# Kernel tuning notes

Measured on AMD Instinct MI355X. Metric: run time of the kernel, lower is better.

The kernel has to match this reference:

```python
import jax, jax.numpy as jnp
import numpy as np
import math

B, S, KV, D, H = 4, 512, 4096, 1024, 16
HD = D // H  # head_dim = 64


def setup_inputs() -> dict:
    key = jax.random.key(0)
    ks = jax.random.split(key, 12)
    scale = 0.02
    return {
        "x": jax.random.normal(ks[0], (B, S, D), dtype=jnp.float32),
        "xa": jax.random.normal(ks[1], (B, KV, D), dtype=jnp.float32),
        "Wq": jax.random.normal(ks[2], (D, D), dtype=jnp.float32) * scale,
        "bq": jax.random.normal(ks[3], (D,), dtype=jnp.float32) * scale,
        "Wk": jax.random.normal(ks[4], (D, D), dtype=jnp.float32) * scale,  # key has no bias
        "Wv": jax.random.normal(ks[5], (D, D), dtype=jnp.float32) * scale,
        "bv": jax.random.normal(ks[6], (D,), dtype=jnp.float32) * scale,
        "Wo": jax.random.normal(ks[7], (D, D), dtype=jnp.float32) * scale,
        "bo": jax.random.normal(ks[8], (D,), dtype=jnp.float32) * scale,
        "cache_k": jnp.zeros((B, H, KV, HD), dtype=jnp.float32),
        "cache_v": jnp.zeros((B, H, KV, HD), dtype=jnp.float32),
    }


def reference(x, xa, Wq, bq, Wk, Wv, bv, Wo, bo, cache_k, cache_v):
    bsz, seq_len, _ = x.shape
    kv_len = xa.shape[1]
    # projections (torch nn.Linear convention: y = x @ W^T + b)
    q = (x @ Wq.T + bq).reshape(bsz, seq_len, H, HD).transpose(0, 2, 1, 3)   # [B,H,S,HD]
    k = (xa @ Wk.T).reshape(bsz, kv_len, H, HD).transpose(0, 2, 1, 3)        # [B,H,KV,HD]
    v = (xa @ Wv.T + bv).reshape(bsz, kv_len, H, HD).transpose(0, 2, 1, 3)   # [B,H,KV,HD]
    # prefill path: scatter k/v into positions [0, kv_len) of the cache
    updated_k = cache_k.at[:, :, :kv_len, :].set(k)
    updated_v = cache_v.at[:, :, :kv_len, :].set(v)
    # attention over full cache, fp32 softmax as in the original
    scores = jnp.einsum('bhqd,bhkd->bhqk', q, updated_k) / math.sqrt(HD)
    probs = jax.nn.softmax(scores.astype(jnp.float32), axis=-1).astype(q.dtype)
    attn = jnp.einsum('bhqk,bhkd->bhqd', probs, updated_v)                   # [B,H,S,HD]
    attn = attn.transpose(0, 2, 1, 3).reshape(bsz, seq_len, H * HD)
    out = attn @ Wo.T + bo
    return out, updated_k, updated_v
```

## Files before the change

### kernel.cpp

```cpp
#include <hip/hip_runtime.h>
#include <hip/hip_bf16.h>

using u16 = unsigned short;
typedef __bf16 bf16x8 __attribute__((ext_vector_type(8)));
typedef float f32x4 __attribute__((ext_vector_type(4)));

#define SB 4
#define SS 512
#define SKV 4096
#define SD 1024
#define SH 16
#define SHD 64
#define NSPLIT 4
#define NROWS 32768

__device__ inline u16 f2bf(float f){
  __hip_bfloat16 h = __float2bfloat16(f);
  return __builtin_bit_cast(u16, h);
}

__device__ inline bf16x8 ld_frag_g(const u16* p){
  uint4 v = *reinterpret_cast<const uint4*>(p);
  return __builtin_bit_cast(bf16x8, v);
}

__device__ inline bf16x8 ld_frag_lds(const char* base, int ob){
  uint4 v = *reinterpret_cast<const uint4*>(base + ob);
  return __builtin_bit_cast(bf16x8, v);
}

__global__ __launch_bounds__(256) void cast_kernel(const float* __restrict__ src,
                                                   u16* __restrict__ dst, int n4){
  int i = blockIdx.x * 256 + threadIdx.x;
  if (i < n4){
    float4 f = reinterpret_cast<const float4*>(src)[i];
    ushort4 u;
    u.x = f2bf(f.x); u.y = f2bf(f.y); u.z = f2bf(f.z); u.w = f2bf(f.w);
    reinterpret_cast<ushort4*>(dst)[i] = u;
  }
}

enum { MODE_Q = 0, MODE_K = 1, MODE_V = 2, MODE_OUT = 3 };

template<int MODE>
__global__ __launch_bounds__(256) void gemm_bt(const u16* __restrict__ A,
                                               const u16* __restrict__ W,
                                               const float* __restrict__ bias,
                                               float* __restrict__ outF,
                                               u16* __restrict__ outB)
{
  __shared__ u16 As[128*64];
  __shared__ u16 Bs[128*64];
  const int tid  = threadIdx.x;
  const int lane = tid & 63;
  const int wm   = ((tid >> 6) >> 1) * 64;
  const int wn   = ((tid >> 6) & 1) * 64;
  const long rowBase = (long)blockIdx.x * 128;
  const long colBase = (long)blockIdx.y * 128;

  f32x4 acc[4][4];
#pragma unroll
  for (int i = 0; i < 4; i++)
#pragma unroll
    for (int j = 0; j < 4; j++)
      acc[i][j] = (f32x4){0.f, 0.f, 0.f, 0.f};

  for (int kt = 0; kt < 16; ++kt){
    __syncthreads();
#pragma unroll
    for (int i = 0; i < 4; i++){
      int u = tid + i * 256;
      int r = u >> 3, c = u & 7;
      uint4 va = *reinterpret_cast<const uint4*>(A + (rowBase + r) * 1024 + kt * 64 + c * 8);
      uint4 vw = *reinterpret_cast<const uint4*>(W + (colBase + r) * 1024 + kt * 64 + c * 8);
      int ob = (r * 128 + c * 16) ^ ((r & 7) << 4);
      *reinterpret_cast<uint4*>(reinterpret_cast<char*>(As) + ob) = va;
      *reinterpret_cast<uint4*>(reinterpret_cast<char*>(Bs) + ob) = vw;
    }
    __syncthreads();
#pragma unroll
    for (int kk = 0; kk < 2; kk++){
      bf16x8 af[4], bfr[4];
#pragma unroll
      for (int mi = 0; mi < 4; mi++){
        int row = wm + mi * 16 + (lane & 15);
        int ob = (row * 128 + kk * 64 + (lane >> 4) * 16) ^ ((row & 7) << 4);
        af[mi] = __builtin_bit_cast(bf16x8,
                 *reinterpret_cast<const uint4*>(reinterpret_cast<const char*>(As) + ob));
      }
#pragma unroll
      for (int ni = 0; ni < 4; ni++){
        int row = wn + ni * 16 + (lane & 15);
        int ob = (row * 128 + kk * 64 + (lane >> 4) * 16) ^ ((row & 7) << 4);
        bfr[ni] = __builtin_bit_cast(bf16x8,
                 *reinterpret_cast<const uint4*>(reinterpret_cast<const char*>(Bs) + ob));
      }
#pragma unroll
      for (int mi = 0; mi < 4; mi++)
#pragma unroll
        for (int ni = 0; ni < 4; ni++)
          acc[mi][ni] = __builtin_amdgcn_mfma_f32_16x16x32_bf16(af[mi], bfr[ni], acc[mi][ni], 0, 0, 0);
    }
  }

#pragma unroll
  for (int mi = 0; mi < 4; mi++){
#pragma unroll
    for (int ni = 0; ni < 4; ni++){
      long gn = colBase + wn + ni * 16 + (lane & 15);
      float bb = 0.f;
      if (MODE == MODE_Q || MODE == MODE_V || MODE == MODE_OUT) bb = bias[gn];
      if (MODE == MODE_V){
        long gmBase = rowBase + wm + mi * 16 + ((lane >> 4) << 2);
        long b = gmBase >> 12, kv = gmBase & 4095;
        long h = gn >> 6, hd = gn & 63;
        long fidx = ((b * SH + h) * SKV + kv) * SHD + hd;
        ushort4 pk;
        float v0 = acc[mi][ni][0] + bb; outF[fidx          ] = v0; pk.x = f2bf(v0);
        float v1 = acc[mi][ni][1] + bb; outF[fidx +     SHD] = v1; pk.y = f2bf(v1);
        float v2 = acc[mi][ni][2] + bb; outF[fidx + 2 * SHD] = v2; pk.z = f2bf(v2);
        float v3 = acc[mi][ni][3] + bb; outF[fidx + 3 * SHD] = v3; pk.w = f2bf(v3);
        *reinterpret_cast<ushort4*>(outB + ((b * SH + h) * SHD + hd) * SKV + kv) = pk;
      } else {
#pragma unroll
        for (int r = 0; r < 4; r++){
          long gm = rowBase + wm + mi * 16 + ((lane >> 4) << 2) + r;
          float val = acc[mi][ni][r] + bb;
          if (MODE == MODE_OUT){
            outF[gm * 1024 + gn] = val;
          } else if (MODE == MODE_Q){
            long b = gm >> 9, s = gm & 511;
            long h = gn >> 6, hd = gn & 63;
            outB[((b * SH + h) * SS + s) * SHD + hd] = f2bf(val);
          } else {
            long b = gm >> 12, kv = gm & 4095;
            long h = gn >> 6, hd = gn & 63;
            long idx = ((b * SH + h) * SKV + kv) * SHD + hd;
            outF[idx] = val;
            outB[idx] = f2bf(val);
          }
        }
      }
    }
  }
}

__global__ __launch_bounds__(256) void attn_partial(const u16* __restrict__ qb,
                                                    const u16* __restrict__ kb,
                                                    const u16* __restrict__ vTb,
                                                    float* __restrict__ opart,
                                                    float* __restrict__ ml){
  __shared__ u16 Klds[64 * 64];
  __shared__ u16 Vlds[64 * 64];
  __shared__ u16 PT[4][16 * 72];
  const int tid  = threadIdx.x;
  const int lane = tid & 63;
  const int wid  = tid >> 6;
  const int c    = lane & 15;
  const int hi   = lane >> 4;
  const long bh  = blockIdx.x;
  const int  qt  = blockIdx.y;
  const int  split = blockIdx.z;

  const u16* qp = qb + (bh * SS + qt * 64 + wid * 16 + c) * SHD + hi * 8;
  const bf16x8 bq0 = ld_frag_g(qp);
  const bf16x8 bq1 = ld_frag_g(qp + 32);

  f32x4 acc[4];
#pragma unroll
  for (int i = 0; i < 4; i++) acc[i] = (f32x4){0.f, 0.f, 0.f, 0.f};
  float mrun = -INFINITY, lrun = 0.f;

  const u16* kbase = kb  + bh * SKV * SHD;
  const u16* vbase = vTb + bh * SHD * SKV;
  u16* pt = &PT[wid][0];
  char* kch = reinterpret_cast<char*>(Klds);
  char* vch = reinterpret_cast<char*>(Vlds);

  for (int kt = split * 16; kt < split * 16 + 16; ++kt){
    __syncthreads();
#pragma unroll
    for (int i = 0; i < 2; i++){
      int u = tid + i * 256;
      int r = u >> 3, cc = u & 7;
      uint4 kv4 = *reinterpret_cast<const uint4*>(kbase + (kt * 64 + r) * SHD + cc * 8);
      uint4 vv4 = *reinterpret_cast<const uint4*>(vbase + (long)r * SKV + kt * 64 + cc * 8);
      int ob = (r * 128 + cc * 16) ^ ((r & 7) << 4);
      *reinterpret_cast<uint4*>(kch + ob) = kv4;
      *reinterpret_cast<uint4*>(vch + ob) = vv4;
    }
    __syncthreads();

    f32x4 sT[4];
#pragma unroll
    for (int ni = 0; ni < 4; ni++){
      int krow = ni * 16 + c;
      int swz = (krow & 7) << 4;
      int a0 = (krow * 128 + hi * 16) ^ swz;
      int a1 = (krow * 128 + 64 + hi * 16) ^ swz;
      f32x4 z = (f32x4){0.f, 0.f, 0.f, 0.f};
      sT[ni] = __builtin_amdgcn_mfma_f32_16x16x32_bf16(ld_frag_lds(kch, a0), bq0, z, 0, 0, 0);
      sT[ni] = __builtin_amdgcn_mfma_f32_16x16x32_bf16(ld_frag_lds(kch, a1), bq1, sT[ni], 0, 0, 0);
      sT[ni] *= 0.125f;
    }
    f32x4 mv = __builtin_elementwise_max(__builtin_elementwise_max(sT[0], sT[1]),
                                         __builtin_elementwise_max(sT[2], sT[3]));
    float t = fmaxf(fmaxf(mv[0], mv[1]), fmaxf(mv[2], mv[3]));
    t = fmaxf(t, __shfl_xor(t, 16));
    t = fmaxf(t, __shfl_xor(t, 32));
    float mn = fmaxf(mrun, t);
    float al = __expf(mrun - mn);
    f32x4 psv = (f32x4){0.f, 0.f, 0.f, 0.f};
#pragma unroll
    for (int ni = 0; ni < 4; ni++){
      f32x4 p;
      p[0] = __expf(sT[ni][0] - mn); p[1] = __expf(sT[ni][1] - mn);
      p[2] = __expf(sT[ni][2] - mn); p[3] = __expf(sT[ni][3] - mn);
      psv += p;
      ushort4 pk;
      pk.x = f2bf(p[0]); pk.y = f2bf(p[1]); pk.z = f2bf(p[2]); pk.w = f2bf(p[3]);
      *reinterpret_cast<ushort4*>(pt + c * 72 + ni * 16 + hi * 4) = pk;
    }
    float ps = (psv[0] + psv[1]) + (psv[2] + psv[3]);
    ps += __shfl_xor(ps, 16);
    ps += __shfl_xor(ps, 32);
    lrun = lrun * al + ps;
    mrun = mn;
#pragma unroll
    for (int ni = 0; ni < 4; ni++) acc[ni] *= al;
#pragma unroll
    for (int m = 0; m < 2; m++){
      bf16x8 pfrag = __builtin_bit_cast(bf16x8,
          *reinterpret_cast<const uint4*>(pt + c * 72 + m * 32 + hi * 8));
#pragma unroll
      for (int ni = 0; ni < 4; ni++){
        int vrow = ni * 16 + c;
        int av = (vrow * 128 + m * 64 + hi * 16) ^ ((vrow & 7) << 4);
        acc[ni] = __builtin_amdgcn_mfma_f32_16x16x32_bf16(ld_frag_lds(vch, av), pfrag, acc[ni], 0, 0, 0);
      }
    }
  }

  const long row = bh * SS + (long)qt * 64 + wid * 16 + c;
  float* ob = opart + ((long)split * NROWS + row) * SHD;
#pragma unroll
  for (int ni = 0; ni < 4; ni++)
    *reinterpret_cast<f32x4*>(ob + ni * 16 + hi * 4) = acc[ni];
  if (hi == 0){
    ml[(long)split * NROWS + row] = mrun;
    ml[(long)NSPLIT * NROWS + (long)split * NROWS + row] = lrun;
  }
}

__global__ __launch_bounds__(256) void attn_combine(const float* __restrict__ opart,
                                                    const float* __restrict__ ml,
                                                    u16* __restrict__ attnb){
  long idx4 = (long)blockIdx.x * 256 + threadIdx.x;
  long row = idx4 >> 4;
  int  c   = (int)(idx4 & 15);
  float m0 = ml[row], m1 = ml[NROWS + row], m2 = ml[2L*NROWS + row], m3 = ml[3L*NROWS + row];
  float M = fmaxf(fmaxf(m0, m1), fmaxf(m2, m3));
  float w0 = __expf(m0 - M), w1 = __expf(m1 - M), w2 = __expf(m2 - M), w3 = __expf(m3 - M);
  const float* lb = ml + (long)NSPLIT * NROWS;
  float L = w0*lb[row] + w1*lb[NROWS+row] + w2*lb[2L*NROWS+row] + w3*lb[3L*NROWS+row];
  float inv = 1.f / L;
  const float4* op = reinterpret_cast<const float4*>(opart);
  float4 v0 = op[(0L*NROWS + row) * 16 + c];
  float4 v1 = op[(1L*NROWS + row) * 16 + c];
  float4 v2 = op[(2L*NROWS + row) * 16 + c];
  float4 v3 = op[(3L*NROWS + row) * 16 + c];
  float4 val;
  val.x = (w0*v0.x + w1*v1.x + w2*v2.x + w3*v3.x) * inv;
  val.y = (w0*v0.y + w1*v1.y + w2*v2.y + w3*v3.y) * inv;
  val.z = (w0*v0.z + w1*v1.z + w2*v2.z + w3*v3.z) * inv;
  val.w = (w0*v0.w + w1*v1.w + w2*v2.w + w3*v3.w) * inv;
  long bh = row >> 9, s = row & 511;
  long b = bh >> 4, h = bh & 15;
  ushort4 u;
  u.x = f2bf(val.x); u.y = f2bf(val.y); u.z = f2bf(val.z); u.w = f2bf(val.w);
  reinterpret_cast<ushort4*>(attnb)[((b * SS + s) * SD + h * SHD) / 4 + c] = u;
}

extern "C" void kernel_launch(void* const* d_in, const int* in_sizes, int n_in,
                              void* d_out, int out_size, void* d_ws, size_t ws_size,
                              hipStream_t stream)
{
  const float* x  = (const float*)d_in[0];
  const float* xa = (const float*)d_in[1];
  const float* Wq = (const float*)d_in[2];
  const float* bq = (const float*)d_in[3];
  const float* Wk = (const float*)d_in[4];
  const float* Wv = (const float*)d_in[5];
  const float* bv = (const float*)d_in[6];
  const float* Wo = (const float*)d_in[7];
  const float* bo = (const float*)d_in[8];

  float* outO = (float*)d_out;
  float* outK = outO + (long)SB * SS * SD;
  float* outV = outK + (long)SB * SH * SKV * SHD;

  u16* ws   = (u16*)d_ws;
  u16* xb   = ws;
  u16* xab  = xb   + 2097152L;
  u16* Wqb  = xab  + 16777216L;
  u16* Wkb  = Wqb  + 1048576L;
  u16* Wvb  = Wkb  + 1048576L;
  u16* Wob  = Wvb  + 1048576L;
  u16* qbuf = Wob  + 1048576L;
  u16* kbuf = qbuf + 2097152L;
  u16* vTbuf= kbuf + 16777216L;
  u16* mlb  = vTbuf+ 16777216L;

  u16*   attnb = xb;
  float* opart = (float*)xab;
  float* ml    = (float*)mlb;

  auto cast_launch = [&](const float* s, u16* d, long n){
    int n4 = (int)(n / 4);
    cast_kernel<<<(n4 + 255) / 256, 256, 0, stream>>>(s, d, n4);
  };
  cast_launch(x,  xb,  2097152L);
  cast_launch(xa, xab, 16777216L);
  cast_launch(Wq, Wqb, 1048576L);
  cast_launch(Wk, Wkb, 1048576L);
  cast_launch(Wv, Wvb, 1048576L);
  cast_launch(Wo, Wob, 1048576L);

  gemm_bt<MODE_Q>  <<<dim3(16, 8),  256, 0, stream>>>(xb,  Wqb, bq, nullptr, qbuf);
  gemm_bt<MODE_K>  <<<dim3(128, 8), 256, 0, stream>>>(xab, Wkb, nullptr, outK, kbuf);
  gemm_bt<MODE_V>  <<<dim3(128, 8), 256, 0, stream>>>(xab, Wvb, bv, outV, vTbuf);
  attn_partial     <<<dim3(64, 8, NSPLIT), 256, 0, stream>>>(qbuf, kbuf, vTbuf, opart, ml);
  attn_combine     <<<2048, 256, 0, stream>>>(opart, ml, attnb);
  gemm_bt<MODE_OUT><<<dim3(16, 8),  256, 0, stream>>>(attnb, Wob, bo, outO, nullptr);
}
```

Measured before the change: 275.0 us.

## Fuse K and V projections into one GEMM and fold softmax scale into Q

Replaces the separate K and V projection GEMMs with a single kernel that loads each xa tile once and computes both outputs with two accumulator sets. It also folds the 1/sqrt(HD) scale and log2(e) into the Q projection so attention can use exp2f without a per-score multiply. The goal is to halve the reads of the large bf16 xa activation and trim ALU work in the softmax loop. In exchange the fused kernel doubles its accumulator registers and LDS footprint, which may lower occupancy, and pre-scaling Q before the bf16 cast slightly changes rounding.

Measured after the change: 301.4 us. +9.6%, slower.

```diff
diff --git a/kernel.cpp b/kernel.cpp
--- a/kernel.cpp
+++ b/kernel.cpp
@@ -13,6 +13,7 @@
 #define SHD 64
 #define NSPLIT 4
 #define NROWS 32768
+#define QSCALE 0.18033688011112042f
 
 __device__ inline u16 f2bf(float f){
   __hip_bfloat16 h = __float2bfloat16(f);
@@ -40,7 +41,7 @@
   }
 }
 
-enum { MODE_Q = 0, MODE_K = 1, MODE_V = 2, MODE_OUT = 3 };
+enum { MODE_Q = 0, MODE_OUT = 3 };
 
 template<int MODE>
 __global__ __launch_bounds__(256) void gemm_bt(const u16* __restrict__ A,
@@ -85,15 +86,13 @@
       for (int mi = 0; mi < 4; mi++){
         int row = wm + mi * 16 + (lane & 15);
         int ob = (row * 128 + kk * 64 + (lane >> 4) * 16) ^ ((row & 7) << 4);
-        af[mi] = __builtin_bit_cast(bf16x8,
-                 *reinterpret_cast<const uint4*>(reinterpret_cast<const char*>(As) + ob));
+        af[mi] = ld_frag_lds(reinterpret_cast<const char*>(As), ob);
       }
 #pragma unroll
       for (int ni = 0; ni < 4; ni++){
         int row = wn + ni * 16 + (lane & 15);
         int ob = (row * 128 + kk * 64 + (lane >> 4) * 16) ^ ((row & 7) << 4);
-        bfr[ni] = __builtin_bit_cast(bf16x8,
-                 *reinterpret_cast<const uint4*>(reinterpret_cast<const char*>(Bs) + ob));
+        bfr[ni] = ld_frag_lds(reinterpret_cast<const char*>(Bs), ob);
       }
 #pragma unroll
       for (int mi = 0; mi < 4; mi++)
@@ -108,39 +107,117 @@
 #pragma unroll
     for (int ni = 0; ni < 4; ni++){
       long gn = colBase + wn + ni * 16 + (lane & 15);
-      float bb = 0.f;
-      if (MODE == MODE_Q || MODE == MODE_V || MODE == MODE_OUT) bb = bias[gn];
-      if (MODE == MODE_V){
-        long gmBase = rowBase + wm + mi * 16 + ((lane >> 4) << 2);
-        long b = gmBase >> 12, kv = gmBase & 4095;
-        long h = gn >> 6, hd = gn & 63;
-        long fidx = ((b * SH + h) * SKV + kv) * SHD + hd;
-        ushort4 pk;
-        float v0 = acc[mi][ni][0] + bb; outF[fidx          ] = v0; pk.x = f2bf(v0);
-        float v1 = acc[mi][ni][1] + bb; outF[fidx +     SHD] = v1; pk.y = f2bf(v1);
-        float v2 = acc[mi][ni][2] + bb; outF[fidx + 2 * SHD] = v2; pk.z = f2bf(v2);
-        float v3 = acc[mi][ni][3] + bb; outF[fidx + 3 * SHD] = v3; pk.w = f2bf(v3);
-        *reinterpret_cast<ushort4*>(outB + ((b * SH + h) * SHD + hd) * SKV + kv) = pk;
-      } else {
-#pragma unroll
-        for (int r = 0; r < 4; r++){
-          long gm = rowBase + wm + mi * 16 + ((lane >> 4) << 2) + r;
-          float val = acc[mi][ni][r] + bb;
-          if (MODE == MODE_OUT){
-            outF[gm * 1024 + gn] = val;
-          } else if (MODE == MODE_Q){
-            long b = gm >> 9, s = gm & 511;
-            long h = gn >> 6, hd = gn & 63;
-            outB[((b * SH + h) * SS + s) * SHD + hd] = f2bf(val);
-          } else {
-            long b = gm >> 12, kv = gm & 4095;
-            long h = gn >> 6, hd = gn & 63;
-            long idx = ((b * SH + h) * SKV + kv) * SHD + hd;
-            outF[idx] = val;
-            outB[idx] = f2bf(val);
-          }
+      float bb = bias[gn];
+#pragma unroll
+      for (int r = 0; r < 4; r++){
+        long gm = rowBase + wm + mi * 16 + ((lane >> 4) << 2) + r;
+        float val = acc[mi][ni][r] + bb;
+        if (MODE == MODE_OUT){
+          outF[gm * 1024 + gn] = val;
+        } else {
+          long b = gm >> 9, s = gm & 511;
+          long h = gn >> 6, hd = gn & 63;
+          outB[((b * SH + h) * SS + s) * SHD + hd] = f2bf(val * QSCALE);
         }
       }
+    }
+  }
+}
+
+__global__ __launch_bounds__(256) void gemm_kv(const u16* __restrict__ A,
+                                               const u16* __restrict__ Wk,
+                                               const u16* __restrict__ Wv,
+                                               const float* __restrict__ bv,
+                                               float* __restrict__ outK,
+                                               u16* __restrict__ outKb,
+                                               float* __restrict__ outV,
+                                               u16* __restrict__ outVTb)
+{
+  __shared__ u16 As [128*64];
+  __shared__ u16 Bks[128*64];
+  __shared__ u16 Bvs[128*64];
+  const int tid  = threadIdx.x;
+  const int lane = tid & 63;
+  const int wm   = ((tid >> 6) >> 1) * 64;
+  const int wn   = ((tid >> 6) & 1) * 64;
+  const long rowBase = (long)blockIdx.x * 128;
+  const long colBase = (long)blockIdx.y * 128;
+
+  f32x4 accK[4][4], accV[4][4];
+#pragma unroll
+  for (int i = 0; i < 4; i++)
+#pragma unroll
+    for (int j = 0; j < 4; j++){
+      accK[i][j] = (f32x4){0.f, 0.f, 0.f, 0.f};
+      accV[i][j] = (f32x4){0.f, 0.f, 0.f, 0.f};
+    }
+
+  for (int kt = 0; kt < 16; ++kt){
+    __syncthreads();
+#pragma unroll
+    for (int i = 0; i < 4; i++){
+      int u = tid + i * 256;
+      int r = u >> 3, c = u & 7;
+      uint4 va = *reinterpret_cast<const uint4*>(A  + (rowBase + r) * 1024 + kt * 64 + c * 8);
+      uint4 vk = *reinterpret_cast<const uint4*>(Wk + (colBase + r) * 1024 + kt * 64 + c * 8);
+      uint4 vv = *reinterpret_cast<const uint4*>(Wv + (colBase + r) * 1024 + kt * 64 + c * 8);
+      int ob = (r * 128 + c * 16) ^ ((r & 7) << 4);
+      *reinterpret_cast<uint4*>(reinterpret_cast<char*>(As)  + ob) = va;
+      *reinterpret_cast<uint4*>(reinterpret_cast<char*>(Bks) + ob) = vk;
+      *reinterpret_cast<uint4*>(reinterpret_cast<char*>(Bvs) + ob) = vv;
+    }
+    __syncthreads();
+#pragma unroll
+    for (int kk = 0; kk < 2; kk++){
+      bf16x8 af[4], bk[4], bvf[4];
+#pragma unroll
+      for (int mi = 0; mi < 4; mi++){
+        int row = wm + mi * 16 + (lane & 15);
+        int ob = (row * 128 + kk * 64 + (lane >> 4) * 16) ^ ((row & 7) << 4);
+        af[mi] = ld_frag_lds(reinterpret_cast<const char*>(As), ob);
+      }
+#pragma unroll
+      for (int ni = 0; ni < 4; ni++){
+        int row = wn + ni * 16 + (lane & 15);
+        int ob = (row * 128 + kk * 64 + (lane >> 4) * 16) ^ ((row & 7) << 4);
+        bk[ni]  = ld_frag_lds(reinterpret_cast<const char*>(Bks), ob);
+        bvf[ni] = ld_frag_lds(reinterpret_cast<const char*>(Bvs), ob);
+      }
+#pragma unroll
+      for (int mi = 0; mi < 4; mi++)
+#pragma unroll
+        for (int ni = 0; ni < 4; ni++){
+          accK[mi][ni] = __builtin_amdgcn_mfma_f32_16x16x32_bf16(af[mi], bk[ni],  accK[mi][ni], 0, 0, 0);
+          accV[mi][ni] = __builtin_amdgcn_mfma_f32_16x16x32_bf16(af[mi], bvf[ni], accV[mi][ni], 0, 0, 0);
+        }
+    }
+  }
+
+#pragma unroll
+  for (int mi = 0; mi < 4; mi++){
+#pragma unroll
+    for (int ni = 0; ni < 4; ni++){
+      long gn = colBase + wn + ni * 16 + (lane & 15);
+      long h = gn >> 6, hd = gn & 63;
+#pragma unroll
+      for (int r = 0; r < 4; r++){
+        long gm = rowBase + wm + mi * 16 + ((lane >> 4) << 2) + r;
+        long b = gm >> 12, kv = gm & 4095;
+        long idx = ((b * SH + h) * SKV + kv) * SHD + hd;
+        float val = accK[mi][ni][r];
+        outK[idx] = val;
+        outKb[idx] = f2bf(val);
+      }
+      float bb = bv[gn];
+      long gmBase = rowBase + wm + mi * 16 + ((lane >> 4) << 2);
+      long b = gmBase >> 12, kv = gmBase & 4095;
+      long fidx = ((b * SH + h) * SKV + kv) * SHD + hd;
+      ushort4 pk;
+      float v0 = accV[mi][ni][0] + bb; outV[fidx          ] = v0; pk.x = f2bf(v0);
+      float v1 = accV[mi][ni][1] + bb; outV[fidx +     SHD] = v1; pk.y = f2bf(v1);
+      float v2 = accV[mi][ni][2] + bb; outV[fidx + 2 * SHD] = v2; pk.z = f2bf(v2);
+      float v3 = accV[mi][ni][3] + bb; outV[fidx + 3 * SHD] = v3; pk.w = f2bf(v3);
+      *reinterpret_cast<ushort4*>(outVTb + ((b * SH + h) * SHD + hd) * SKV + kv) = pk;
     }
   }
 }
@@ -201,7 +278,6 @@
       f32x4 z = (f32x4){0.f, 0.f, 0.f, 0.f};
       sT[ni] = __builtin_amdgcn_mfma_f32_16x16x32_bf16(ld_frag_lds(kch, a0), bq0, z, 0, 0, 0);
       sT[ni] = __builtin_amdgcn_mfma_f32_16x16x32_bf16(ld_frag_lds(kch, a1), bq1, sT[ni], 0, 0, 0);
-      sT[ni] *= 0.125f;
     }
     f32x4 mv = __builtin_elementwise_max(__builtin_elementwise_max(sT[0], sT[1]),
                                          __builtin_elementwise_max(sT[2], sT[3]));
@@ -209,13 +285,13 @@
     t = fmaxf(t, __shfl_xor(t, 16));
     t = fmaxf(t, __shfl_xor(t, 32));
     float mn = fmaxf(mrun, t);
-    float al = __expf(mrun - mn);
+    float al = exp2f(mrun - mn);
     f32x4 psv = (f32x4){0.f, 0.f, 0.f, 0.f};
 #pragma unroll
     for (int ni = 0; ni < 4; ni++){
       f32x4 p;
-      p[0] = __expf(sT[ni][0] - mn); p[1] = __expf(sT[ni][1] - mn);
-      p[2] = __expf(sT[ni][2] - mn); p[3] = __expf(sT[ni][3] - mn);
+      p[0] = exp2f(sT[ni][0] - mn); p[1] = exp2f(sT[ni][1] - mn);
+      p[2] = exp2f(sT[ni][2] - mn); p[3] = exp2f(sT[ni][3] - mn);
       psv += p;
       ushort4 pk;
       pk.x = f2bf(p[0]); pk.y = f2bf(p[1]); pk.z = f2bf(p[2]); pk.w = f2bf(p[3]);
@@ -260,7 +336,7 @@
   int  c   = (int)(idx4 & 15);
   float m0 = ml[row], m1 = ml[NROWS + row], m2 = ml[2L*NROWS + row], m3 = ml[3L*NROWS + row];
   float M = fmaxf(fmaxf(m0, m1), fmaxf(m2, m3));
-  float w0 = __expf(m0 - M), w1 = __expf(m1 - M), w2 = __expf(m2 - M), w3 = __expf(m3 - M);
+  float w0 = exp2f(m0 - M), w1 = exp2f(m1 - M), w2 = exp2f(m2 - M), w3 = exp2f(m3 - M);
   const float* lb = ml + (long)NSPLIT * NROWS;
   float L = w0*lb[row] + w1*lb[NROWS+row] + w2*lb[2L*NROWS+row] + w3*lb[3L*NROWS+row];
   float inv = 1.f / L;
@@ -327,8 +403,8 @@
   cast_launch(Wo, Wob, 1048576L);
 
   gemm_bt<MODE_Q>  <<<dim3(16, 8),  256, 0, stream>>>(xb,  Wqb, bq, nullptr, qbuf);
-  gemm_bt<MODE_K>  <<<dim3(128, 8), 256, 0, stream>>>(xab, Wkb, nullptr, outK, kbuf);
-  gemm_bt<MODE_V>  <<<dim3(128, 8), 256, 0, stream>>>(xab, Wvb, bv, outV, vTbuf);
+  gemm_kv          <<<dim3(128, 8), 256, 0, stream>>>(xab, Wkb, Wvb, bv,
+                                                      outK, kbuf, outV, vTbuf);
   attn_partial     <<<dim3(64, 8, NSPLIT), 256, 0, stream>>>(qbuf, kbuf, vTbuf, opart, ml);
   attn_combine     <<<2048, 256, 0, stream>>>(opart, ml, attnb);
   gemm_bt<MODE_OUT><<<dim3(16, 8),  256, 0, stream>>>(attnb, Wob, bo, outO, nullptr);
```

## Process two query tiles per warp in attention and fold softmax scale into Q

Applied to the files above, without the earlier changes.

Each attention warp now handles 32 query rows instead of 16, so every K and V fragment loaded from LDS feeds two MFMAs. This halves the number of K/V tile loads per query and halves the grid along the query axis. The softmax scale and log2(e) are folded into Q in the projection epilogue, which lets the kernel use exp2f and drop the per-score multiply. The price is more registers per thread and fewer blocks (1024 instead of 2048), so occupancy may drop; Q is also rounded to bf16 after scaling, which changes rounding slightly.

Measured after the change: 283.9 us. 1.03x slower.

```diff
diff --git a/kernel.cpp b/kernel.cpp
--- a/kernel.cpp
+++ b/kernel.cpp
@@ -13,6 +13,7 @@
 #define SHD 64
 #define NSPLIT 4
 #define NROWS 32768
+#define QSCALE 0.18033688011112042f
 
 __device__ inline u16 f2bf(float f){
   __hip_bfloat16 h = __float2bfloat16(f);
@@ -85,15 +86,13 @@
       for (int mi = 0; mi < 4; mi++){
         int row = wm + mi * 16 + (lane & 15);
         int ob = (row * 128 + kk * 64 + (lane >> 4) * 16) ^ ((row & 7) << 4);
-        af[mi] = __builtin_bit_cast(bf16x8,
-                 *reinterpret_cast<const uint4*>(reinterpret_cast<const char*>(As) + ob));
+        af[mi] = ld_frag_lds(reinterpret_cast<const char*>(As), ob);
       }
 #pragma unroll
       for (int ni = 0; ni < 4; ni++){
         int row = wn + ni * 16 + (lane & 15);
         int ob = (row * 128 + kk * 64 + (lane >> 4) * 16) ^ ((row & 7) << 4);
-        bfr[ni] = __builtin_bit_cast(bf16x8,
-                 *reinterpret_cast<const uint4*>(reinterpret_cast<const char*>(Bs) + ob));
+        bfr[ni] = ld_frag_lds(reinterpret_cast<const char*>(Bs), ob);
       }
 #pragma unroll
       for (int mi = 0; mi < 4; mi++)
@@ -131,7 +130,7 @@
           } else if (MODE == MODE_Q){
             long b = gm >> 9, s = gm & 511;
             long h = gn >> 6, hd = gn & 63;
-            outB[((b * SH + h) * SS + s) * SHD + hd] = f2bf(val);
+            outB[((b * SH + h) * SS + s) * SHD + hd] = f2bf(val * QSCALE);
           } else {
             long b = gm >> 12, kv = gm & 4095;
             long h = gn >> 6, hd = gn & 63;
@@ -152,7 +151,7 @@
                                                     float* __restrict__ ml){
   __shared__ u16 Klds[64 * 64];
   __shared__ u16 Vlds[64 * 64];
-  __shared__ u16 PT[4][16 * 72];
+  __shared__ u16 PT[4][32 * 72];
   const int tid  = threadIdx.x;
   const int lane = tid & 63;
   const int wid  = tid >> 6;
@@ -162,14 +161,20 @@
   const int  qt  = blockIdx.y;
   const int  split = blockIdx.z;
 
-  const u16* qp = qb + (bh * SS + qt * 64 + wid * 16 + c) * SHD + hi * 8;
+  const u16* qp = qb + (bh * SS + qt * 128 + wid * 32 + c) * SHD + hi * 8;
   const bf16x8 bq0 = ld_frag_g(qp);
   const bf16x8 bq1 = ld_frag_g(qp + 32);
-
-  f32x4 acc[4];
-#pragma unroll
-  for (int i = 0; i < 4; i++) acc[i] = (f32x4){0.f, 0.f, 0.f, 0.f};
-  float mrun = -INFINITY, lrun = 0.f;
+  const bf16x8 bq2 = ld_frag_g(qp + 16 * SHD);
+  const bf16x8 bq3 = ld_frag_g(qp + 16 * SHD + 32);
+
+  f32x4 acc0[4], acc1[4];
+#pragma unroll
+  for (int i = 0; i < 4; i++){
+    acc0[i] = (f32x4){0.f, 0.f, 0.f, 0.f};
+    acc1[i] = (f32x4){0.f, 0.f, 0.f, 0.f};
+  }
+  float mrun0 = -INFINITY, lrun0 = 0.f;
+  float mrun1 = -INFINITY, lrun1 = 0.f;
 
   const u16* kbase = kb  + bh * SKV * SHD;
   const u16* vbase = vTb + bh * SHD * SKV;
@@ -191,64 +196,81 @@
     }
     __syncthreads();
 
-    f32x4 sT[4];
+    f32x4 sT0[4], sT1[4];
 #pragma unroll
     for (int ni = 0; ni < 4; ni++){
       int krow = ni * 16 + c;
       int swz = (krow & 7) << 4;
-      int a0 = (krow * 128 + hi * 16) ^ swz;
-      int a1 = (krow * 128 + 64 + hi * 16) ^ swz;
+      bf16x8 kf0 = ld_frag_lds(kch, (krow * 128 + hi * 16) ^ swz);
+      bf16x8 kf1 = ld_frag_lds(kch, (krow * 128 + 64 + hi * 16) ^ swz);
       f32x4 z = (f32x4){0.f, 0.f, 0.f, 0.f};
-      sT[ni] = __builtin_amdgcn_mfma_f32_16x16x32_bf16(ld_frag_lds(kch, a0), bq0, z, 0, 0, 0);
-      sT[ni] = __builtin_amdgcn_mfma_f32_16x16x32_bf16(ld_frag_lds(kch, a1), bq1, sT[ni], 0, 0, 0);
-      sT[ni] *= 0.125f;
-    }
-    f32x4 mv = __builtin_elementwise_max(__builtin_elementwise_max(sT[0], sT[1]),
-                                         __builtin_elementwise_max(sT[2], sT[3]));
-    float t = fmaxf(fmaxf(mv[0], mv[1]), fmaxf(mv[2], mv[3]));
-    t = fmaxf(t, __shfl_xor(t, 16));
-    t = fmaxf(t, __shfl_xor(t, 32));
-    float mn = fmaxf(mrun, t);
-    float al = __expf(mrun - mn);
-    f32x4 psv = (f32x4){0.f, 0.f, 0.f, 0.f};
-#pragma unroll
-    for (int ni = 0; ni < 4; ni++){
-      f32x4 p;
-      p[0] = __expf(sT[ni][0] - mn); p[1] = __expf(sT[ni][1] - mn);
-      p[2] = __expf(sT[ni][2] - mn); p[3] = __expf(sT[ni][3] - mn);
-      psv += p;
-      ushort4 pk;
-      pk.x = f2bf(p[0]); pk.y = f2bf(p[1]); pk.z = f2bf(p[2]); pk.w = f2bf(p[3]);
-      *reinterpret_cast<ushort4*>(pt + c * 72 + ni * 16 + hi * 4) = pk;
-    }
-    float ps = (psv[0] + psv[1]) + (psv[2] + psv[3]);
-    ps += __shfl_xor(ps, 16);
-    ps += __shfl_xor(ps, 32);
-    lrun = lrun * al + ps;
-    mrun = mn;
-#pragma unroll
-    for (int ni = 0; ni < 4; ni++) acc[ni] *= al;
+      sT0[ni] = __builtin_amdgcn_mfma_f32_16x16x32_bf16(kf0, bq0, z, 0, 0, 0);
+      sT0[ni] = __builtin_amdgcn_mfma_f32_16x16x32_bf16(kf1, bq1, sT0[ni], 0, 0, 0);
+      sT1[ni] = __builtin_amdgcn_mfma_f32_16x16x32_bf16(kf0, bq2, z, 0, 0, 0);
+      sT1[ni] = __builtin_amdgcn_mfma_f32_16x16x32_bf16(kf1, bq3, sT1[ni], 0, 0, 0);
+    }
+#pragma unroll
+    for (int g = 0; g < 2; g++){
+      f32x4* sT = g ? sT1 : sT0;
+      f32x4* ac = g ? acc1 : acc0;
+      float& mrun = g ? mrun1 : mrun0;
+      float& lrun = g ? lrun1 : lrun0;
+      f32x4 mv = __builtin_elementwise_max(__builtin_elementwise_max(sT[0], sT[1]),
+                                           __builtin_elementwise_max(sT[2], sT[3]));
+      float t = fmaxf(fmaxf(mv[0], mv[1]), fmaxf(mv[2], mv[3]));
+      t = fmaxf(t, __shfl_xor(t, 16));
+      t = fmaxf(t, __shfl_xor(t, 32));
+      float mn = fmaxf(mrun, t);
+      float al = exp2f(mrun - mn);
+      f32x4 psv = (f32x4){0.f, 0.f, 0.f, 0.f};
+#pragma unroll
+      for (int ni = 0; ni < 4; ni++){
+        f32x4 p;
+        p[0] = exp2f(sT[ni][0] - mn); p[1] = exp2f(sT[ni][1] - mn);
+        p[2] = exp2f(sT[ni][2] - mn); p[3] = exp2f(sT[ni][3] - mn);
+        psv += p;
+        ushort4 pk;
+        pk.x = f2bf(p[0]); pk.y = f2bf(p[1]); pk.z = f2bf(p[2]); pk.w = f2bf(p[3]);
+        *reinterpret_cast<ushort4*>(pt + (c + g * 16) * 72 + ni * 16 + hi * 4) = pk;
+      }
+      float ps = (psv[0] + psv[1]) + (psv[2] + psv[3]);
+      ps += __shfl_xor(ps, 16);
+      ps += __shfl_xor(ps, 32);
+      lrun = lrun * al + ps;
+      mrun = mn;
+#pragma unroll
+      for (int ni = 0; ni < 4; ni++) ac[ni] *= al;
+    }
 #pragma unroll
     for (int m = 0; m < 2; m++){
-      bf16x8 pfrag = __builtin_bit_cast(bf16x8,
+      bf16x8 pf0 = __builtin_bit_cast(bf16x8,
           *reinterpret_cast<const uint4*>(pt + c * 72 + m * 32 + hi * 8));
+      bf16x8 pf1 = __builtin_bit_cast(bf16x8,
+          *reinterpret_cast<const uint4*>(pt + (c + 16) * 72 + m * 32 + hi * 8));
 #pragma unroll
       for (int ni = 0; ni < 4; ni++){
         int vrow = ni * 16 + c;
-        int av = (vrow * 128 + m * 64 + hi * 16) ^ ((vrow & 7) << 4);
-        acc[ni] = __builtin_amdgcn_mfma_f32_16x16x32_bf16(ld_frag_lds(vch, av), pfrag, acc[ni], 0, 0, 0);
-      }
-    }
-  }
-
-  const long row = bh * SS + (long)qt * 64 + wid * 16 + c;
-  float* ob = opart + ((long)split * NROWS + row) * SHD;
-#pragma unroll
-  for (int ni = 0; ni < 4; ni++)
-    *reinterpret_cast<f32x4*>(ob + ni * 16 + hi * 4) = acc[ni];
+        bf16x8 vf = ld_frag_lds(vch, (vrow * 128 + m * 64 + hi * 16) ^ ((vrow & 7) << 4));
+        acc0[ni] = __builtin_amdgcn_mfma_f32_16x16x32_bf16(vf, pf0, acc0[ni], 0, 0, 0);
+        acc1[ni] = __builtin_amdgcn_mfma_f32_16x16x32_bf16(vf, pf1, acc1[ni], 0, 0, 0);
+      }
+    }
+  }
+
+  const long row0 = bh * SS + (long)qt * 128 + wid * 32 + c;
+  const long row1 = row0 + 16;
+  float* ob0 = opart + ((long)split * NROWS + row0) * SHD;
+  float* ob1 = opart + ((long)split * NROWS + row1) * SHD;
+#pragma unroll
+  for (int ni = 0; ni < 4; ni++){
+    *reinterpret_cast<f32x4*>(ob0 + ni * 16 + hi * 4) = acc0[ni];
+    *reinterpret_cast<f32x4*>(ob1 + ni * 16 + hi * 4) = acc1[ni];
+  }
   if (hi == 0){
-    ml[(long)split * NROWS + row] = mrun;
-    ml[(long)NSPLIT * NROWS + (long)split * NROWS + row] = lrun;
+    ml[(long)split * NROWS + row0] = mrun0;
+    ml[(long)NSPLIT * NROWS + (long)split * NROWS + row0] = lrun0;
+    ml[(long)split * NROWS + row1] = mrun1;
+    ml[(long)NSPLIT * NROWS + (long)split * NROWS + row1] = lrun1;
   }
 }
 
@@ -260,7 +282,7 @@
   int  c   = (int)(idx4 & 15);
   float m0 = ml[row], m1 = ml[NROWS + row], m2 = ml[2L*NROWS + row], m3 = ml[3L*NROWS + row];
   float M = fmaxf(fmaxf(m0, m1), fmaxf(m2, m3));
-  float w0 = __expf(m0 - M), w1 = __expf(m1 - M), w2 = __expf(m2 - M), w3 = __expf(m3 - M);
+  float w0 = exp2f(m0 - M), w1 = exp2f(m1 - M), w2 = exp2f(m2 - M), w3 = exp2f(m3 - M);
   const float* lb = ml + (long)NSPLIT * NROWS;
   float L = w0*lb[row] + w1*lb[NROWS+row] + w2*lb[2L*NROWS+row] + w3*lb[3L*NROWS+row];
   float inv = 1.f / L;
@@ -329,7 +351,7 @@
   gemm_bt<MODE_Q>  <<<dim3(16, 8),  256, 0, stream>>>(xb,  Wqb, bq, nullptr, qbuf);
   gemm_bt<MODE_K>  <<<dim3(128, 8), 256, 0, stream>>>(xab, Wkb, nullptr, outK, kbuf);
   gemm_bt<MODE_V>  <<<dim3(128, 8), 256, 0, stream>>>(xab, Wvb, bv, outV, vTbuf);
-  attn_partial     <<<dim3(64, 8, NSPLIT), 256, 0, stream>>>(qbuf, kbuf, vTbuf, opart, ml);
+  attn_partial     <<<dim3(64, 4, NSPLIT), 256, 0, stream>>>(qbuf, kbuf, vTbuf, opart, ml);
   attn_combine     <<<2048, 256, 0, stream>>>(opart, ml, attnb);
   gemm_bt<MODE_OUT><<<dim3(16, 8),  256, 0, stream>>>(attnb, Wob, bo, outO, nullptr);
 }
```
